# Kernel tuning notes

Hardware: AMD Instinct MI355X
Metric: run time of the kernel (lower is better)

The kernel has to match this reference:

```python
import jax, jax.numpy as jnp
import numpy as np

N_ENT, N_REL, DIM, L, B, M = 500000, 32, 64, 2, 2048, 64


def setup_inputs() -> dict:
    key = jax.random.key(0)
    ks = jax.random.split(key, 16)
    f = lambda k, shape: (jax.random.normal(k, shape, jnp.float32) * 0.05)
    inp = {
        "ent_emb": f(ks[0], (N_ENT, DIM)),
        "rec_emb": f(ks[1], (N_ENT, DIM)),
        "rel_emb": f(ks[2], (N_REL, DIM)),
        "w1": f(ks[3], (DIM, 2 * DIM)), "b1": jnp.zeros((DIM,), jnp.float32),
        "w2": f(ks[4], (DIM, DIM)), "b2": jnp.zeros((DIM,), jnp.float32),
        "w3": f(ks[5], (1, DIM)), "b3": jnp.zeros((1,), jnp.float32),
        "wagg": f(ks[6], (DIM, (L + 1) * DIM)), "bagg": jnp.zeros((DIM,), jnp.float32),
        "u_ent": jax.random.randint(ks[7], (B, M), 0, N_ENT),
        "u_heads": jax.random.randint(ks[8], (L, B, M), 0, N_ENT),
        "u_rels": jax.random.randint(ks[9], (L, B, M), 0, N_REL),
        "u_tails": jax.random.randint(ks[10], (L, B, M), 0, N_ENT),
        "v_ent": jax.random.randint(ks[11], (B, M), 0, N_ENT),
        "v_heads": jax.random.randint(ks[12], (L, B, M), 0, N_ENT),
        "v_rels": jax.random.randint(ks[13], (L, B, M), 0, N_REL),
        "v_tails": jax.random.randint(ks[14], (L, B, M), 0, N_ENT),
    }
    return inp


def _dnn(x, w1, b1, w2, b2, w3, b3):
    # x: [B, M, 2*DIM] -> [B, M, 1], matches torch DNN (relu, relu, sigmoid)
    y = jax.nn.relu(x @ w1.T + b1)
    y = jax.nn.relu(y @ w2.T + b2)
    return jax.nn.sigmoid(y @ w3.T + b3)


def _side(emb0_table, ent_emb, rel_emb, ent, heads, rels, tails,
          w1, b1, w2, b2, w3, b3, wagg, bagg):
    e_list = [emb0_table[ent].mean(axis=1)]  # hop-0: [B, DIM]
    for l in range(L):
        h = ent_emb[heads[l]]            # [B, M, DIM]
        r = rel_emb[rels[l]]             # [B, M, DIM]
        pi = _dnn(jnp.concatenate([h, r], axis=-1), w1, b1, w2, b2, w3, b3)
        pi = jax.nn.softmax(pi, axis=1)  # softmax over neighbor set
        a = (pi * ent_emb[tails[l]]).sum(axis=1)  # [B, DIM]
        e_list.append(a)
    emb = jnp.concatenate(e_list, axis=-1)  # [B, (L+1)*DIM]
    return jax.nn.sigmoid(emb @ wagg.T + bagg)  # agg == 'concat'


def reference(ent_emb, rec_emb, rel_emb, w1, b1, w2, b2, w3, b3, wagg, bagg,
              u_ent, u_heads, u_rels, u_tails, v_ent, v_heads, v_rels, v_tails):
    users = _side(rec_emb, ent_emb, rel_emb, u_ent, u_heads, u_rels, u_tails,
                  w1, b1, w2, b2, w3, b3, wagg, bagg)
    items = _side(ent_emb, ent_emb, rel_emb, v_ent, v_heads, v_rels, v_tails,
                  w1, b1, w2, b2, w3, b3, wagg, bagg)
    return jax.nn.sigmoid((users * items).sum(axis=1))  # [B]
```

## Files before the change

kernel.cpp:

```cpp
#include <hip/hip_runtime.h>
#include <math.h>

#define BB 2048
#define MM 64

typedef __attribute__((ext_vector_type(8))) short short8;
typedef __attribute__((ext_vector_type(4))) float float4v;
typedef __attribute__((ext_vector_type(4))) int int4v;

union Frag { int4v v; short8 s; int u[4]; };

#define OFF_A1    0
#define OFF_A2    4096
#define OFF_WAGGT 6144
#define OFF_EP    18432

__device__ __forceinline__ float sigmoidf_(float x) {
    return 1.0f / (1.0f + expf(-x));
}

__device__ __forceinline__ int pk2(float lo, float hi) {
    int r;
    asm("v_cvt_pk_bf16_f32 %0, %1, %2" : "=v"(r) : "v"(lo), "v"(hi));
    return r;
}

__global__ __launch_bounds__(256) void prep_kernel(
    const float* __restrict__ w1, const float* __restrict__ w2,
    const float* __restrict__ wagg, int* __restrict__ wsI) {
    int t = blockIdx.x * 256 + threadIdx.x;
    if (t < 4096) {
        int r = t & 3, lane = (t >> 2) & 63, ks = (t >> 8) & 3, tr = t >> 10;
        int j = tr * 16 + (lane & 15);
        int k = ks * 32 + (lane >> 4) * 8 + 2 * r;
        wsI[OFF_A1 + t] = pk2(w1[j * 128 + k], w1[j * 128 + k + 1]);
    }
    if (t < 2048) {
        int r = t & 3, lane = (t >> 2) & 63, ks = (t >> 8) & 1, tr = t >> 9;
        int j = tr * 16 + (lane & 15);
        int k = ks * 32 + (lane >> 4) * 8 + 2 * r;
        wsI[OFF_A2 + t] = pk2(w2[j * 64 + k], w2[j * 64 + k + 1]);
    }
    if (t < 12288) {
        int k = t >> 6, j = t & 63;
        ((float*)wsI)[OFF_WAGGT + t] = wagg[j * 192 + k];
    }
}

__global__ __launch_bounds__(256) void hop0_kernel(
    const float* __restrict__ ent_emb, const float* __restrict__ rec_emb,
    const int* __restrict__ u_ent, const int* __restrict__ v_ent,
    float* __restrict__ e_parts) {
    int wt = blockIdx.x * 4 + (threadIdx.x >> 6);
    int lane = threadIdx.x & 63;
    int b = wt & 2047;
    int side = wt >> 11;
    const int* ent = side ? v_ent : u_ent;
    const float* tab = side ? ent_emb : rec_emb;
    float a0 = 0.f, a1 = 0.f, a2 = 0.f, a3 = 0.f;
#pragma unroll 4
    for (int m = 0; m < 64; m += 4) {
        int e0 = ent[b * 64 + m + 0], e1 = ent[b * 64 + m + 1];
        int e2 = ent[b * 64 + m + 2], e3 = ent[b * 64 + m + 3];
        a0 += tab[(size_t)e0 * 64 + lane];
        a1 += tab[(size_t)e1 * 64 + lane];
        a2 += tab[(size_t)e2 * 64 + lane];
        a3 += tab[(size_t)e3 * 64 + lane];
    }
    e_parts[((side * 3 + 0) * BB + b) * 64 + lane] =
        (a0 + a1 + a2 + a3) * (1.0f / 64.0f);
}

__global__ __launch_bounds__(256) void attn_kernel(
    const float* __restrict__ ent_emb, const float* __restrict__ rel_emb,
    const float* __restrict__ b1, const float* __restrict__ b2,
    const float* __restrict__ w3, const float* __restrict__ b3,
    const int* __restrict__ u_heads, const int* __restrict__ u_rels,
    const int* __restrict__ u_tails,
    const int* __restrict__ v_heads, const int* __restrict__ v_rels,
    const int* __restrict__ v_tails,
    const int* __restrict__ wsI, float* __restrict__ e_parts) {
    int lane = threadIdx.x & 63;
    int wt = blockIdx.x * 4 + (threadIdx.x >> 6);
    int b = wt & 2047;
    int l = (wt >> 11) & 1;
    int side = wt >> 12;
    int c = lane & 15, g = lane >> 4;

    const int* heads = side ? v_heads : u_heads;
    const int* rels  = side ? v_rels  : u_rels;
    const int* tails = side ? v_tails : u_tails;
    int base = (l * BB + b) * MM + lane;
    int hidx = heads[base];
    int ridx = rels[base];
    int tidx = tails[base];

    const int4v* a1p = (const int4v*)(wsI + OFF_A1);
    const int4v* a2p = (const int4v*)(wsI + OFF_A2);

    Frag bx[4][4];
#pragma unroll
    for (int tc = 0; tc < 4; tc++) {
        int hn = __shfl(hidx, tc * 16 + c);
        int rn = __shfl(ridx, tc * 16 + c);
        const float4v* hp = (const float4v*)(ent_emb + (size_t)hn * 64 + g * 8);
        const float4v* rp = (const float4v*)(rel_emb + (size_t)rn * 64 + g * 8);
        float4v h0 = hp[0], h1 = hp[1], h2 = hp[8], h3 = hp[9];
        float4v r0 = rp[0], r1 = rp[1], r2 = rp[8], r3 = rp[9];
        bx[tc][0].u[0] = pk2(h0[0], h0[1]); bx[tc][0].u[1] = pk2(h0[2], h0[3]);
        bx[tc][0].u[2] = pk2(h1[0], h1[1]); bx[tc][0].u[3] = pk2(h1[2], h1[3]);
        bx[tc][1].u[0] = pk2(h2[0], h2[1]); bx[tc][1].u[1] = pk2(h2[2], h2[3]);
        bx[tc][1].u[2] = pk2(h3[0], h3[1]); bx[tc][1].u[3] = pk2(h3[2], h3[3]);
        bx[tc][2].u[0] = pk2(r0[0], r0[1]); bx[tc][2].u[1] = pk2(r0[2], r0[3]);
        bx[tc][2].u[2] = pk2(r1[0], r1[1]); bx[tc][2].u[3] = pk2(r1[2], r1[3]);
        bx[tc][3].u[0] = pk2(r2[0], r2[1]); bx[tc][3].u[1] = pk2(r2[2], r2[3]);
        bx[tc][3].u[2] = pk2(r3[0], r3[1]); bx[tc][3].u[3] = pk2(r3[2], r3[3]);
    }

    float4v acc[4][4];
#pragma unroll
    for (int tr = 0; tr < 4; tr++) {
        float4v bias = *(const float4v*)(b1 + tr * 16 + g * 4);
        Frag a1s[4];
#pragma unroll
        for (int ks = 0; ks < 4; ks++)
            a1s[ks].v = a1p[(tr * 4 + ks) * 64 + lane];
#pragma unroll
        for (int tc = 0; tc < 4; tc++) {
            float4v cacc = bias;
#pragma unroll
            for (int ks = 0; ks < 4; ks++)
                cacc = __builtin_amdgcn_mfma_f32_16x16x32_bf16(
                    a1s[ks].s, bx[tc][ks].s, cacc, 0, 0, 0);
            acc[tr][tc] = cacc;
        }
    }

    Frag b2f[4][2];
#pragma unroll
    for (int tc = 0; tc < 4; tc++) {
        int pk[4][2];
#pragma unroll
        for (int trp = 0; trp < 4; trp++) {
#pragma unroll
            for (int ip = 0; ip < 2; ip++) {
                float lo = fmaxf(acc[trp][tc][2 * ip], 0.0f);
                float hi = fmaxf(acc[trp][tc][2 * ip + 1], 0.0f);
                pk[trp][ip] = pk2(lo, hi);
            }
        }
#pragma unroll
        for (int ks2 = 0; ks2 < 2; ks2++) {
#pragma unroll
            for (int r = 0; r < 4; r++) {
                int srclane = (lane & 15) | ((lane & 16) << 1) | ((r >> 1) << 4);
                int va = __shfl(pk[2 * ks2 + 0][r & 1], srclane);
                int vb = __shfl(pk[2 * ks2 + 1][r & 1], srclane);
                b2f[tc][ks2].u[r] = (lane & 32) ? vb : va;
            }
        }
    }

    float4v acc2[4][4];
#pragma unroll
    for (int tr = 0; tr < 4; tr++) {
        float4v bias = *(const float4v*)(b2 + tr * 16 + g * 4);
        Frag a2s[2];
#pragma unroll
        for (int ks = 0; ks < 2; ks++)
            a2s[ks].v = a2p[(tr * 2 + ks) * 64 + lane];
#pragma unroll
        for (int tc = 0; tc < 4; tc++) {
            float4v cacc = bias;
#pragma unroll
            for (int ks = 0; ks < 2; ks++)
                cacc = __builtin_amdgcn_mfma_f32_16x16x32_bf16(
                    a2s[ks].s, b2f[tc][ks].s, cacc, 0, 0, 0);
            acc2[tr][tc] = cacc;
        }
    }

    float4v w3f[4];
#pragma unroll
    for (int tr = 0; tr < 4; tr++)
        w3f[tr] = *(const float4v*)(w3 + tr * 16 + g * 4);
    float b3v = b3[0];

    float pv[4];
#pragma unroll
    for (int tc = 0; tc < 4; tc++) {
        float pt = 0.0f;
#pragma unroll
        for (int tr = 0; tr < 4; tr++) {
#pragma unroll
            for (int i = 0; i < 4; i++)
                pt = fmaf(fmaxf(acc2[tr][tc][i], 0.0f), w3f[tr][i], pt);
        }
        pt += __shfl_xor(pt, 16);
        pt += __shfl_xor(pt, 32);
        pv[tc] = sigmoidf_(pt + b3v);
    }

    float mx = fmaxf(fmaxf(pv[0], pv[1]), fmaxf(pv[2], pv[3]));
#pragma unroll
    for (int o = 1; o < 16; o <<= 1) mx = fmaxf(mx, __shfl_xor(mx, o));
    float ex[4];
    float sm = 0.0f;
#pragma unroll
    for (int tc = 0; tc < 4; tc++) { ex[tc] = expf(pv[tc] - mx); sm += ex[tc]; }
#pragma unroll
    for (int o = 1; o < 16; o <<= 1) sm += __shfl_xor(sm, o);
    float inv = 1.0f / sm;
    float p[4];
#pragma unroll
    for (int tc = 0; tc < 4; tc++) p[tc] = ex[tc] * inv;

    float pa0 = 0.f, pa1 = 0.f, pa2 = 0.f, pa3 = 0.f;
#pragma unroll 4
    for (int m = 0; m < 64; m += 4) {
        float pm0 = __shfl(p[(m + 0) >> 4], (m + 0) & 15);
        float pm1 = __shfl(p[(m + 1) >> 4], (m + 1) & 15);
        float pm2 = __shfl(p[(m + 2) >> 4], (m + 2) & 15);
        float pm3 = __shfl(p[(m + 3) >> 4], (m + 3) & 15);
        int tm0 = __shfl(tidx, m + 0), tm1 = __shfl(tidx, m + 1);
        int tm2 = __shfl(tidx, m + 2), tm3 = __shfl(tidx, m + 3);
        pa0 = fmaf(pm0, ent_emb[(size_t)tm0 * 64 + lane], pa0);
        pa1 = fmaf(pm1, ent_emb[(size_t)tm1 * 64 + lane], pa1);
        pa2 = fmaf(pm2, ent_emb[(size_t)tm2 * 64 + lane], pa2);
        pa3 = fmaf(pm3, ent_emb[(size_t)tm3 * 64 + lane], pa3);
    }
    e_parts[((side * 3 + (l + 1)) * BB + b) * 64 + lane] =
        pa0 + pa1 + pa2 + pa3;
}

__global__ __launch_bounds__(256) void final_kernel(
    const float* __restrict__ bagg, const float* __restrict__ wsF,
    float* __restrict__ out) {
    const float* waggT = wsF + OFF_WAGGT;
    const float* ep = wsF + OFF_EP;
    int b = blockIdx.x * 4 + (threadIdx.x >> 6);
    int lane = threadIdx.x & 63;
    float eu[3], ev[3];
#pragma unroll
    for (int cc = 0; cc < 3; cc++) {
        eu[cc] = ep[((0 * 3 + cc) * BB + b) * 64 + lane];
        ev[cc] = ep[((1 * 3 + cc) * BB + b) * 64 + lane];
    }
    float us = bagg[lane], it = bagg[lane];
#pragma unroll
    for (int k = 0; k < 192; k++) {
        float w = waggT[k * 64 + lane];
        us = fmaf(__shfl(eu[k >> 6], k & 63), w, us);
        it = fmaf(__shfl(ev[k >> 6], k & 63), w, it);
    }
    us = sigmoidf_(us);
    it = sigmoidf_(it);
    float prod = us * it;
#pragma unroll
    for (int o = 32; o > 0; o >>= 1) prod += __shfl_xor(prod, o);
    if (lane == 0) out[b] = sigmoidf_(prod);
}

extern "C" void kernel_launch(void* const* d_in, const int* in_sizes, int n_in,
                              void* d_out, int out_size, void* d_ws, size_t ws_size,
                              hipStream_t stream) {
    const float* ent_emb = (const float*)d_in[0];
    const float* rec_emb = (const float*)d_in[1];
    const float* rel_emb = (const float*)d_in[2];
    const float* w1   = (const float*)d_in[3];
    const float* b1   = (const float*)d_in[4];
    const float* w2   = (const float*)d_in[5];
    const float* b2   = (const float*)d_in[6];
    const float* w3   = (const float*)d_in[7];
    const float* b3   = (const float*)d_in[8];
    const float* wagg = (const float*)d_in[9];
    const float* bagg = (const float*)d_in[10];
    const int* u_ent   = (const int*)d_in[11];
    const int* u_heads = (const int*)d_in[12];
    const int* u_rels  = (const int*)d_in[13];
    const int* u_tails = (const int*)d_in[14];
    const int* v_ent   = (const int*)d_in[15];
    const int* v_heads = (const int*)d_in[16];
    const int* v_rels  = (const int*)d_in[17];
    const int* v_tails = (const int*)d_in[18];

    int* wsI = (int*)d_ws;
    float* wsF = (float*)d_ws;
    float* e_parts = wsF + OFF_EP;
    float* out = (float*)d_out;

    prep_kernel<<<48, 256, 0, stream>>>(w1, w2, wagg, wsI);
    hop0_kernel<<<1024, 256, 0, stream>>>(ent_emb, rec_emb, u_ent, v_ent, e_parts);
    attn_kernel<<<2048, 256, 0, stream>>>(ent_emb, rel_emb, b1, b2, w3, b3,
                                          u_heads, u_rels, u_tails,
                                          v_heads, v_rels, v_tails,
                                          wsI, e_parts);
    final_kernel<<<512, 256, 0, stream>>>(bagg, wsF, out);
}
```

Measured before the change: 326.5 us.

## Fuse hop0 into attention kernel and stream DNN per column tile

Merges the hop-0 mean-gather kernel into the attention kernel as extra blocks, removing one launch and letting both gather workloads overlap. The DNN is restructured to process one 16-neighbor column tile at a time instead of holding all four tiles' fragments and accumulators, cutting register pressure, and launch bounds now request 8 blocks per CU. The gather loops are unrolled to 8 independent loads to raise memory-level parallelism, and hop0 indices are loaded once per lane and broadcast by shuffle. The risk is less MFMA interleaving across tiles and heterogeneous blocks within one grid.

```diff
diff --git a/kernel.cpp b/kernel.cpp
--- a/kernel.cpp
+++ b/kernel.cpp
@@ -47,41 +47,50 @@
     }
 }
 
-__global__ __launch_bounds__(256) void hop0_kernel(
+__global__ __launch_bounds__(256, 8) void fused_kernel(
     const float* __restrict__ ent_emb, const float* __restrict__ rec_emb,
-    const int* __restrict__ u_ent, const int* __restrict__ v_ent,
-    float* __restrict__ e_parts) {
-    int wt = blockIdx.x * 4 + (threadIdx.x >> 6);
-    int lane = threadIdx.x & 63;
-    int b = wt & 2047;
-    int side = wt >> 11;
-    const int* ent = side ? v_ent : u_ent;
-    const float* tab = side ? ent_emb : rec_emb;
-    float a0 = 0.f, a1 = 0.f, a2 = 0.f, a3 = 0.f;
-#pragma unroll 4
-    for (int m = 0; m < 64; m += 4) {
-        int e0 = ent[b * 64 + m + 0], e1 = ent[b * 64 + m + 1];
-        int e2 = ent[b * 64 + m + 2], e3 = ent[b * 64 + m + 3];
-        a0 += tab[(size_t)e0 * 64 + lane];
-        a1 += tab[(size_t)e1 * 64 + lane];
-        a2 += tab[(size_t)e2 * 64 + lane];
-        a3 += tab[(size_t)e3 * 64 + lane];
-    }
-    e_parts[((side * 3 + 0) * BB + b) * 64 + lane] =
-        (a0 + a1 + a2 + a3) * (1.0f / 64.0f);
-}
-
-__global__ __launch_bounds__(256) void attn_kernel(
-    const float* __restrict__ ent_emb, const float* __restrict__ rel_emb,
+    const float* __restrict__ rel_emb,
     const float* __restrict__ b1, const float* __restrict__ b2,
     const float* __restrict__ w3, const float* __restrict__ b3,
+    const int* __restrict__ u_ent, const int* __restrict__ v_ent,
     const int* __restrict__ u_heads, const int* __restrict__ u_rels,
     const int* __restrict__ u_tails,
     const int* __restrict__ v_heads, const int* __restrict__ v_rels,
     const int* __restrict__ v_tails,
     const int* __restrict__ wsI, float* __restrict__ e_parts) {
     int lane = threadIdx.x & 63;
-    int wt = blockIdx.x * 4 + (threadIdx.x >> 6);
+    int wv = threadIdx.x >> 6;
+
+    if (blockIdx.x >= 2048) {
+        int wt = (blockIdx.x - 2048) * 4 + wv;
+        int b = wt & 2047;
+        int side = wt >> 11;
+        const int* ent = side ? v_ent : u_ent;
+        const float* tab = side ? ent_emb : rec_emb;
+        int em = ent[b * 64 + lane];
+        float s0 = 0.f, s1 = 0.f, s2 = 0.f, s3 = 0.f;
+        float s4 = 0.f, s5 = 0.f, s6 = 0.f, s7 = 0.f;
+#pragma unroll
+        for (int m = 0; m < 64; m += 8) {
+            int e0 = __shfl(em, m + 0), e1 = __shfl(em, m + 1);
+            int e2 = __shfl(em, m + 2), e3 = __shfl(em, m + 3);
+            int e4 = __shfl(em, m + 4), e5 = __shfl(em, m + 5);
+            int e6 = __shfl(em, m + 6), e7 = __shfl(em, m + 7);
+            s0 += tab[(size_t)e0 * 64 + lane];
+            s1 += tab[(size_t)e1 * 64 + lane];
+            s2 += tab[(size_t)e2 * 64 + lane];
+            s3 += tab[(size_t)e3 * 64 + lane];
+            s4 += tab[(size_t)e4 * 64 + lane];
+            s5 += tab[(size_t)e5 * 64 + lane];
+            s6 += tab[(size_t)e6 * 64 + lane];
+            s7 += tab[(size_t)e7 * 64 + lane];
+        }
+        float s = ((s0 + s1) + (s2 + s3)) + ((s4 + s5) + (s6 + s7));
+        e_parts[((side * 3 + 0) * BB + b) * 64 + lane] = s * (1.0f / 64.0f);
+        return;
+    }
+
+    int wt = blockIdx.x * 4 + wv;
     int b = wt & 2047;
     int l = (wt >> 11) & 1;
     int side = wt >> 12;
@@ -97,58 +106,52 @@
 
     const int4v* a1p = (const int4v*)(wsI + OFF_A1);
     const int4v* a2p = (const int4v*)(wsI + OFF_A2);
-
-    Frag bx[4][4];
-#pragma unroll
-    for (int tc = 0; tc < 4; tc++) {
+    float b3v = b3[0];
+
+    auto dnn_tc = [&](const int tc) -> float {
         int hn = __shfl(hidx, tc * 16 + c);
         int rn = __shfl(ridx, tc * 16 + c);
         const float4v* hp = (const float4v*)(ent_emb + (size_t)hn * 64 + g * 8);
         const float4v* rp = (const float4v*)(rel_emb + (size_t)rn * 64 + g * 8);
         float4v h0 = hp[0], h1 = hp[1], h2 = hp[8], h3 = hp[9];
         float4v r0 = rp[0], r1 = rp[1], r2 = rp[8], r3 = rp[9];
-        bx[tc][0].u[0] = pk2(h0[0], h0[1]); bx[tc][0].u[1] = pk2(h0[2], h0[3]);
-        bx[tc][0].u[2] = pk2(h1[0], h1[1]); bx[tc][0].u[3] = pk2(h1[2], h1[3]);
-        bx[tc][1].u[0] = pk2(h2[0], h2[1]); bx[tc][1].u[1] = pk2(h2[2], h2[3]);
-        bx[tc][1].u[2] = pk2(h3[0], h3[1]); bx[tc][1].u[3] = pk2(h3[2], h3[3]);
-        bx[tc][2].u[0] = pk2(r0[0], r0[1]); bx[tc][2].u[1] = pk2(r0[2], r0[3]);
-        bx[tc][2].u[2] = pk2(r1[0], r1[1]); bx[tc][2].u[3] = pk2(r1[2], r1[3]);
-        bx[tc][3].u[0] = pk2(r2[0], r2[1]); bx[tc][3].u[1] = pk2(r2[2], r2[3]);
-        bx[tc][3].u[2] = pk2(r3[0], r3[1]); bx[tc][3].u[3] = pk2(r3[2], r3[3]);
-    }
-
-    float4v acc[4][4];
-#pragma unroll
-    for (int tr = 0; tr < 4; tr++) {
-        float4v bias = *(const float4v*)(b1 + tr * 16 + g * 4);
-        Frag a1s[4];
-#pragma unroll
-        for (int ks = 0; ks < 4; ks++)
-            a1s[ks].v = a1p[(tr * 4 + ks) * 64 + lane];
-#pragma unroll
-        for (int tc = 0; tc < 4; tc++) {
-            float4v cacc = bias;
-#pragma unroll
-            for (int ks = 0; ks < 4; ks++)
-                cacc = __builtin_amdgcn_mfma_f32_16x16x32_bf16(
-                    a1s[ks].s, bx[tc][ks].s, cacc, 0, 0, 0);
-            acc[tr][tc] = cacc;
-        }
-    }
-
-    Frag b2f[4][2];
-#pragma unroll
-    for (int tc = 0; tc < 4; tc++) {
+        Frag bx0, bx1, bx2, bx3;
+        bx0.u[0] = pk2(h0[0], h0[1]); bx0.u[1] = pk2(h0[2], h0[3]);
+        bx0.u[2] = pk2(h1[0], h1[1]); bx0.u[3] = pk2(h1[2], h1[3]);
+        bx1.u[0] = pk2(h2[0], h2[1]); bx1.u[1] = pk2(h2[2], h2[3]);
+        bx1.u[2] = pk2(h3[0], h3[1]); bx1.u[3] = pk2(h3[2], h3[3]);
+        bx2.u[0] = pk2(r0[0], r0[1]); bx2.u[1] = pk2(r0[2], r0[3]);
+        bx2.u[2] = pk2(r1[0], r1[1]); bx2.u[3] = pk2(r1[2], r1[3]);
+        bx3.u[0] = pk2(r2[0], r2[1]); bx3.u[1] = pk2(r2[2], r2[3]);
+        bx3.u[2] = pk2(r3[0], r3[1]); bx3.u[3] = pk2(r3[2], r3[3]);
+
+        float4v acc[4];
+#pragma unroll
+        for (int tr = 0; tr < 4; tr++) {
+            float4v cacc = *(const float4v*)(b1 + tr * 16 + g * 4);
+            Frag aA, aB, aC, aD;
+            aA.v = a1p[(tr * 4 + 0) * 64 + lane];
+            aB.v = a1p[(tr * 4 + 1) * 64 + lane];
+            aC.v = a1p[(tr * 4 + 2) * 64 + lane];
+            aD.v = a1p[(tr * 4 + 3) * 64 + lane];
+            cacc = __builtin_amdgcn_mfma_f32_16x16x32_bf16(aA.s, bx0.s, cacc, 0, 0, 0);
+            cacc = __builtin_amdgcn_mfma_f32_16x16x32_bf16(aB.s, bx1.s, cacc, 0, 0, 0);
+            cacc = __builtin_amdgcn_mfma_f32_16x16x32_bf16(aC.s, bx2.s, cacc, 0, 0, 0);
+            cacc = __builtin_amdgcn_mfma_f32_16x16x32_bf16(aD.s, bx3.s, cacc, 0, 0, 0);
+            acc[tr] = cacc;
+        }
+
         int pk[4][2];
 #pragma unroll
         for (int trp = 0; trp < 4; trp++) {
 #pragma unroll
             for (int ip = 0; ip < 2; ip++) {
-                float lo = fmaxf(acc[trp][tc][2 * ip], 0.0f);
-                float hi = fmaxf(acc[trp][tc][2 * ip + 1], 0.0f);
+                float lo = fmaxf(acc[trp][2 * ip], 0.0f);
+                float hi = fmaxf(acc[trp][2 * ip + 1], 0.0f);
                 pk[trp][ip] = pk2(lo, hi);
             }
         }
+        Frag b2f[2];
 #pragma unroll
         for (int ks2 = 0; ks2 < 2; ks2++) {
 #pragma unroll
@@ -156,81 +159,78 @@
                 int srclane = (lane & 15) | ((lane & 16) << 1) | ((r >> 1) << 4);
                 int va = __shfl(pk[2 * ks2 + 0][r & 1], srclane);
                 int vb = __shfl(pk[2 * ks2 + 1][r & 1], srclane);
-                b2f[tc][ks2].u[r] = (lane & 32) ? vb : va;
+                b2f[ks2].u[r] = (lane & 32) ? vb : va;
             }
         }
-    }
-
-    float4v acc2[4][4];
-#pragma unroll
-    for (int tr = 0; tr < 4; tr++) {
-        float4v bias = *(const float4v*)(b2 + tr * 16 + g * 4);
-        Frag a2s[2];
-#pragma unroll
-        for (int ks = 0; ks < 2; ks++)
-            a2s[ks].v = a2p[(tr * 2 + ks) * 64 + lane];
-#pragma unroll
-        for (int tc = 0; tc < 4; tc++) {
-            float4v cacc = bias;
-#pragma unroll
-            for (int ks = 0; ks < 2; ks++)
-                cacc = __builtin_amdgcn_mfma_f32_16x16x32_bf16(
-                    a2s[ks].s, b2f[tc][ks].s, cacc, 0, 0, 0);
-            acc2[tr][tc] = cacc;
-        }
-    }
-
-    float4v w3f[4];
-#pragma unroll
-    for (int tr = 0; tr < 4; tr++)
-        w3f[tr] = *(const float4v*)(w3 + tr * 16 + g * 4);
-    float b3v = b3[0];
-
-    float pv[4];
-#pragma unroll
-    for (int tc = 0; tc < 4; tc++) {
+
+        float4v ac2[4];
+#pragma unroll
+        for (int tr = 0; tr < 4; tr++) {
+            float4v cacc = *(const float4v*)(b2 + tr * 16 + g * 4);
+            Frag aA, aB;
+            aA.v = a2p[(tr * 2 + 0) * 64 + lane];
+            aB.v = a2p[(tr * 2 + 1) * 64 + lane];
+            cacc = __builtin_amdgcn_mfma_f32_16x16x32_bf16(aA.s, b2f[0].s, cacc, 0, 0, 0);
+            cacc = __builtin_amdgcn_mfma_f32_16x16x32_bf16(aB.s, b2f[1].s, cacc, 0, 0, 0);
+            ac2[tr] = cacc;
+        }
+
         float pt = 0.0f;
 #pragma unroll
         for (int tr = 0; tr < 4; tr++) {
+            float4v w3t = *(const float4v*)(w3 + tr * 16 + g * 4);
 #pragma unroll
             for (int i = 0; i < 4; i++)
-                pt = fmaf(fmaxf(acc2[tr][tc][i], 0.0f), w3f[tr][i], pt);
+                pt = fmaf(fmaxf(ac2[tr][i], 0.0f), w3t[i], pt);
         }
         pt += __shfl_xor(pt, 16);
         pt += __shfl_xor(pt, 32);
-        pv[tc] = sigmoidf_(pt + b3v);
-    }
-
-    float mx = fmaxf(fmaxf(pv[0], pv[1]), fmaxf(pv[2], pv[3]));
+        return sigmoidf_(pt + b3v);
+    };
+
+    float pv0 = dnn_tc(0);
+    float pv1 = dnn_tc(1);
+    float pv2 = dnn_tc(2);
+    float pv3 = dnn_tc(3);
+
+    float mx = fmaxf(fmaxf(pv0, pv1), fmaxf(pv2, pv3));
 #pragma unroll
     for (int o = 1; o < 16; o <<= 1) mx = fmaxf(mx, __shfl_xor(mx, o));
-    float ex[4];
-    float sm = 0.0f;
-#pragma unroll
-    for (int tc = 0; tc < 4; tc++) { ex[tc] = expf(pv[tc] - mx); sm += ex[tc]; }
+    float e0 = expf(pv0 - mx), e1 = expf(pv1 - mx);
+    float e2 = expf(pv2 - mx), e3 = expf(pv3 - mx);
+    float sm = (e0 + e1) + (e2 + e3);
 #pragma unroll
     for (int o = 1; o < 16; o <<= 1) sm += __shfl_xor(sm, o);
     float inv = 1.0f / sm;
-    float p[4];
-#pragma unroll
-    for (int tc = 0; tc < 4; tc++) p[tc] = ex[tc] * inv;
-
-    float pa0 = 0.f, pa1 = 0.f, pa2 = 0.f, pa3 = 0.f;
-#pragma unroll 4
-    for (int m = 0; m < 64; m += 4) {
-        float pm0 = __shfl(p[(m + 0) >> 4], (m + 0) & 15);
-        float pm1 = __shfl(p[(m + 1) >> 4], (m + 1) & 15);
-        float pm2 = __shfl(p[(m + 2) >> 4], (m + 2) & 15);
-        float pm3 = __shfl(p[(m + 3) >> 4], (m + 3) & 15);
+    float pA[4] = {e0 * inv, e1 * inv, e2 * inv, e3 * inv};
+
+    float aa0 = 0.f, aa1 = 0.f, aa2 = 0.f, aa3 = 0.f;
+    float aa4 = 0.f, aa5 = 0.f, aa6 = 0.f, aa7 = 0.f;
+#pragma unroll
+    for (int m = 0; m < 64; m += 8) {
+        float pm0 = __shfl(pA[(m + 0) >> 4], (m + 0) & 15);
+        float pm1 = __shfl(pA[(m + 1) >> 4], (m + 1) & 15);
+        float pm2 = __shfl(pA[(m + 2) >> 4], (m + 2) & 15);
+        float pm3 = __shfl(pA[(m + 3) >> 4], (m + 3) & 15);
+        float pm4 = __shfl(pA[(m + 4) >> 4], (m + 4) & 15);
+        float pm5 = __shfl(pA[(m + 5) >> 4], (m + 5) & 15);
+        float pm6 = __shfl(pA[(m + 6) >> 4], (m + 6) & 15);
+        float pm7 = __shfl(pA[(m + 7) >> 4], (m + 7) & 15);
         int tm0 = __shfl(tidx, m + 0), tm1 = __shfl(tidx, m + 1);
         int tm2 = __shfl(tidx, m + 2), tm3 = __shfl(tidx, m + 3);
-        pa0 = fmaf(pm0, ent_emb[(size_t)tm0 * 64 + lane], pa0);
-        pa1 = fmaf(pm1, ent_emb[(size_t)tm1 * 64 + lane], pa1);
-        pa2 = fmaf(pm2, ent_emb[(size_t)tm2 * 64 + lane], pa2);
-        pa3 = fmaf(pm3, ent_emb[(size_t)tm3 * 64 + lane], pa3);
-    }
-    e_parts[((side * 3 + (l + 1)) * BB + b) * 64 + lane] =
-        pa0 + pa1 + pa2 + pa3;
+        int tm4 = __shfl(tidx, m + 4), tm5 = __shfl(tidx, m + 5);
+        int tm6 = __shfl(tidx, m + 6), tm7 = __shfl(tidx, m + 7);
+        aa0 = fmaf(pm0, ent_emb[(size_t)tm0 * 64 + lane], aa0);
+        aa1 = fmaf(pm1, ent_emb[(size_t)tm1 * 64 + lane], aa1);
+        aa2 = fmaf(pm2, ent_emb[(size_t)tm2 * 64 + lane], aa2);
+        aa3 = fmaf(pm3, ent_emb[(size_t)tm3 * 64 + lane], aa3);
+        aa4 = fmaf(pm4, ent_emb[(size_t)tm4 * 64 + lane], aa4);
+        aa5 = fmaf(pm5, ent_emb[(size_t)tm5 * 64 + lane], aa5);
+        aa6 = fmaf(pm6, ent_emb[(size_t)tm6 * 64 + lane], aa6);
+        aa7 = fmaf(pm7, ent_emb[(size_t)tm7 * 64 + lane], aa7);
+    }
+    float s = ((aa0 + aa1) + (aa2 + aa3)) + ((aa4 + aa5) + (aa6 + aa7));
+    e_parts[((side * 3 + (l + 1)) * BB + b) * 64 + lane] = s;
 }
 
 __global__ __launch_bounds__(256) void final_kernel(
@@ -290,10 +290,11 @@
     float* out = (float*)d_out;
 
     prep_kernel<<<48, 256, 0, stream>>>(w1, w2, wagg, wsI);
-    hop0_kernel<<<1024, 256, 0, stream>>>(ent_emb, rec_emb, u_ent, v_ent, e_parts);
-    attn_kernel<<<2048, 256, 0, stream>>>(ent_emb, rel_emb, b1, b2, w3, b3,
-                                          u_heads, u_rels, u_tails,
-                                          v_heads, v_rels, v_tails,
-                                          wsI, e_parts);
+    fused_kernel<<<3072, 256, 0, stream>>>(ent_emb, rec_emb, rel_emb,
+                                           b1, b2, w3, b3,
+                                           u_ent, v_ent,
+                                           u_heads, u_rels, u_tails,
+                                           v_heads, v_rels, v_tails,
+                                           wsI, e_parts);
     final_kernel<<<512, 256, 0, stream>>>(bagg, wsF, out);
 }
```

After: 512.0 us. 56.8% more time.

## Merge hop-0 mean gather into attention kernel and widen gather ILP

Applied to the files above, without the earlier changes.

Folds the hop-0 mean-pooling kernel into the attention kernel as extra blocks, so one launch covers both and the memory-bound hop-0 gathers can overlap with the attention blocks. Hop-0 now loads the index row once per lane and broadcasts it by shuffle instead of issuing scalar index loads, with eight independent accumulators. The tail-weighted gather in attention is unrolled to sixteen outstanding loads per lane to raise memory-level parallelism. The cost is higher register pressure, which could lower occupancy for the attention blocks.

```diff
diff --git a/kernel.cpp b/kernel.cpp
--- a/kernel.cpp
+++ b/kernel.cpp
@@ -47,41 +47,50 @@
     }
 }
 
-__global__ __launch_bounds__(256) void hop0_kernel(
+__global__ __launch_bounds__(256) void fused_kernel(
     const float* __restrict__ ent_emb, const float* __restrict__ rec_emb,
-    const int* __restrict__ u_ent, const int* __restrict__ v_ent,
-    float* __restrict__ e_parts) {
-    int wt = blockIdx.x * 4 + (threadIdx.x >> 6);
-    int lane = threadIdx.x & 63;
-    int b = wt & 2047;
-    int side = wt >> 11;
-    const int* ent = side ? v_ent : u_ent;
-    const float* tab = side ? ent_emb : rec_emb;
-    float a0 = 0.f, a1 = 0.f, a2 = 0.f, a3 = 0.f;
-#pragma unroll 4
-    for (int m = 0; m < 64; m += 4) {
-        int e0 = ent[b * 64 + m + 0], e1 = ent[b * 64 + m + 1];
-        int e2 = ent[b * 64 + m + 2], e3 = ent[b * 64 + m + 3];
-        a0 += tab[(size_t)e0 * 64 + lane];
-        a1 += tab[(size_t)e1 * 64 + lane];
-        a2 += tab[(size_t)e2 * 64 + lane];
-        a3 += tab[(size_t)e3 * 64 + lane];
-    }
-    e_parts[((side * 3 + 0) * BB + b) * 64 + lane] =
-        (a0 + a1 + a2 + a3) * (1.0f / 64.0f);
-}
-
-__global__ __launch_bounds__(256) void attn_kernel(
-    const float* __restrict__ ent_emb, const float* __restrict__ rel_emb,
+    const float* __restrict__ rel_emb,
     const float* __restrict__ b1, const float* __restrict__ b2,
     const float* __restrict__ w3, const float* __restrict__ b3,
+    const int* __restrict__ u_ent, const int* __restrict__ v_ent,
     const int* __restrict__ u_heads, const int* __restrict__ u_rels,
     const int* __restrict__ u_tails,
     const int* __restrict__ v_heads, const int* __restrict__ v_rels,
     const int* __restrict__ v_tails,
     const int* __restrict__ wsI, float* __restrict__ e_parts) {
     int lane = threadIdx.x & 63;
-    int wt = blockIdx.x * 4 + (threadIdx.x >> 6);
+    int wv = threadIdx.x >> 6;
+
+    if (blockIdx.x >= 2048) {
+        int wt = (blockIdx.x - 2048) * 4 + wv;
+        int b = wt & 2047;
+        int side = wt >> 11;
+        const int* ent = side ? v_ent : u_ent;
+        const float* tab = side ? ent_emb : rec_emb;
+        int em = ent[b * 64 + lane];
+        float s0 = 0.f, s1 = 0.f, s2 = 0.f, s3 = 0.f;
+        float s4 = 0.f, s5 = 0.f, s6 = 0.f, s7 = 0.f;
+#pragma unroll
+        for (int m = 0; m < 64; m += 8) {
+            int e0 = __shfl(em, m + 0), e1 = __shfl(em, m + 1);
+            int e2 = __shfl(em, m + 2), e3 = __shfl(em, m + 3);
+            int e4 = __shfl(em, m + 4), e5 = __shfl(em, m + 5);
+            int e6 = __shfl(em, m + 6), e7 = __shfl(em, m + 7);
+            s0 += tab[(size_t)e0 * 64 + lane];
+            s1 += tab[(size_t)e1 * 64 + lane];
+            s2 += tab[(size_t)e2 * 64 + lane];
+            s3 += tab[(size_t)e3 * 64 + lane];
+            s4 += tab[(size_t)e4 * 64 + lane];
+            s5 += tab[(size_t)e5 * 64 + lane];
+            s6 += tab[(size_t)e6 * 64 + lane];
+            s7 += tab[(size_t)e7 * 64 + lane];
+        }
+        float s = ((s0 + s1) + (s2 + s3)) + ((s4 + s5) + (s6 + s7));
+        e_parts[((side * 3 + 0) * BB + b) * 64 + lane] = s * (1.0f / 64.0f);
+        return;
+    }
+
+    int wt = blockIdx.x * 4 + wv;
     int b = wt & 2047;
     int l = (wt >> 11) & 1;
     int side = wt >> 12;
@@ -215,22 +224,26 @@
 #pragma unroll
     for (int tc = 0; tc < 4; tc++) p[tc] = ex[tc] * inv;
 
-    float pa0 = 0.f, pa1 = 0.f, pa2 = 0.f, pa3 = 0.f;
-#pragma unroll 4
-    for (int m = 0; m < 64; m += 4) {
-        float pm0 = __shfl(p[(m + 0) >> 4], (m + 0) & 15);
-        float pm1 = __shfl(p[(m + 1) >> 4], (m + 1) & 15);
-        float pm2 = __shfl(p[(m + 2) >> 4], (m + 2) & 15);
-        float pm3 = __shfl(p[(m + 3) >> 4], (m + 3) & 15);
-        int tm0 = __shfl(tidx, m + 0), tm1 = __shfl(tidx, m + 1);
-        int tm2 = __shfl(tidx, m + 2), tm3 = __shfl(tidx, m + 3);
-        pa0 = fmaf(pm0, ent_emb[(size_t)tm0 * 64 + lane], pa0);
-        pa1 = fmaf(pm1, ent_emb[(size_t)tm1 * 64 + lane], pa1);
-        pa2 = fmaf(pm2, ent_emb[(size_t)tm2 * 64 + lane], pa2);
-        pa3 = fmaf(pm3, ent_emb[(size_t)tm3 * 64 + lane], pa3);
-    }
-    e_parts[((side * 3 + (l + 1)) * BB + b) * 64 + lane] =
-        pa0 + pa1 + pa2 + pa3;
+    float aa[16];
+#pragma unroll
+    for (int i = 0; i < 16; i++) aa[i] = 0.0f;
+#pragma unroll
+    for (int m = 0; m < 64; m += 16) {
+        float pm[16];
+        int tm[16];
+#pragma unroll
+        for (int i = 0; i < 16; i++) {
+            pm[i] = __shfl(p[(m + i) >> 4], (m + i) & 15);
+            tm[i] = __shfl(tidx, m + i);
+        }
+#pragma unroll
+        for (int i = 0; i < 16; i++)
+            aa[i] = fmaf(pm[i], ent_emb[(size_t)tm[i] * 64 + lane], aa[i]);
+    }
+    float s = 0.0f;
+#pragma unroll
+    for (int i = 0; i < 16; i++) s += aa[i];
+    e_parts[((side * 3 + (l + 1)) * BB + b) * 64 + lane] = s;
 }
 
 __global__ __launch_bounds__(256) void final_kernel(
@@ -290,10 +303,11 @@
     float* out = (float*)d_out;
 
     prep_kernel<<<48, 256, 0, stream>>>(w1, w2, wagg, wsI);
-    hop0_kernel<<<1024, 256, 0, stream>>>(ent_emb, rec_emb, u_ent, v_ent, e_parts);
-    attn_kernel<<<2048, 256, 0, stream>>>(ent_emb, rel_emb, b1, b2, w3, b3,
-                                          u_heads, u_rels, u_tails,
-                                          v_heads, v_rels, v_tails,
-                                          wsI, e_parts);
+    fused_kernel<<<3072, 256, 0, stream>>>(ent_emb, rec_emb, rel_emb,
+                                           b1, b2, w3, b3,
+                                           u_ent, v_ent,
+                                           u_heads, u_rels, u_tails,
+                                           v_heads, v_rels, v_tails,
+                                           wsI, e_parts);
     final_kernel<<<512, 256, 0, stream>>>(bagg, wsF, out);
 }
```

Result: slower. 364.7 us (+11.7%).
